# Optimization experiments

Measured on AMD Instinct MI355X. Metric: run time of the kernel, lower is better.

## Reference

```python
import jax, jax.numpy as jnp
import numpy as np

B, C, H, W = 2, 14, 128, 128
LOSS_WEIGHT = 0.5  # output = (1 - loss_weight) * sum of per-(bs,cls) log-Hausdorff losses
BIG = 1e6          # 'infinite' 1D distance for columns with no background pixel


def _edt_sq(is_zero):
    """Exact squared Euclidean distance transform of a [H,W] bool map.

    Returns, for every pixel, the squared distance to the nearest True pixel
    of `is_zero` (0 at True pixels). Matches scipy.ndimage.distance_transform_edt
    squared. Two-phase separable brute force (vectorized, no data loops).
    """
    h, w = is_zero.shape
    ii = jnp.arange(h, dtype=jnp.float32)
    absd = jnp.abs(ii[:, None] - ii[None, :])  # [H(i), H(p)] = |i - p|
    # d1[i, q] = min_{p : is_zero[p, q]} |i - p|   (per-column 1D distance)
    d1 = jnp.min(jnp.where(is_zero[None, :, :], absd[:, :, None], BIG), axis=1)  # [H, W]
    jj = jnp.arange(w, dtype=jnp.float32)
    off = (jj[:, None] - jj[None, :]) ** 2  # [W(q), W(j)] = (q - j)^2
    # sq[i, j] = min_q d1[i, q]^2 + (q - j)^2
    return jnp.min(d1[:, :, None] ** 2 + off[None, :, :], axis=1)  # [H, W]


def _distance_field_sq(img):
    """MONAI HausdorffDTLoss.distance_field squared: (edt(fg)+edt(bg))^2.

    fg_dist and bg_dist have disjoint supports, so (fg+bg)^2 = fg^2 + bg^2.
    Zero field if the image is all-foreground or all-background.
    """
    fg = img > 0.5
    field = _edt_sq(~fg) + _edt_sq(fg)
    valid = jnp.any(fg) & jnp.any(~fg)
    return jnp.where(valid, field, 0.0)


def _edge_mask(m):
    """mask XOR binary_erosion(mask): scipy default cross structuring element,
    border_value=0 (borders erode)."""
    p = jnp.pad(m, 1, constant_values=False)
    er = m & p[:-2, 1:-1] & p[2:, 1:-1] & p[1:-1, :-2] & p[1:-1, 2:]
    return m & ~er


def _pair_loss(stud_logit, seg_s, seg_t, teach_pred):
    # stud_logit: [H,W] float logits of this class; seg_s/seg_t: [H,W] bool
    # class masks; teach_pred: [H,W] teacher argmax labels (int)
    es = _edge_mask(seg_s).astype(stud_logit.dtype)
    et = _edge_mask(seg_t)
    pred = es * stud_logit                                      # edges * logits
    targ = jnp.where(et, teach_pred.astype(stud_logit.dtype), 0.0)  # edges * labels
    pred_dt2 = jax.lax.stop_gradient(_distance_field_sq(pred))  # MONAI detaches dt
    targ_dt2 = jax.lax.stop_gradient(_distance_field_sq(targ))
    hd = jnp.mean((pred - targ) ** 2 * (pred_dt2 + targ_dt2))   # alpha = 2
    return jnp.log(hd + 1.0)                                    # LogHausdorffDTLoss


def reference(logits_student, logits_teacher):
    ps = jnp.argmax(logits_student, axis=1)  # softmax is monotone -> argmax of logits
    pt = jnp.argmax(logits_teacher, axis=1)
    cls = jnp.arange(1, C)                   # classes 1..C-1 (background skipped)
    n = B * (C - 1)
    seg_s = (ps[:, None] == cls[None, :, None, None]).reshape(n, H, W)
    seg_t = (pt[:, None] == cls[None, :, None, None]).reshape(n, H, W)
    stud = logits_student[:, 1:].reshape(n, H, W)
    pt_rep = jnp.broadcast_to(pt[:, None], (B, C - 1, H, W)).reshape(n, H, W)
    losses = jax.vmap(_pair_loss)(stud, seg_s, seg_t, pt_rep)
    return (1.0 - LOSS_WEIGHT) * jnp.sum(losses)


def setup_inputs() -> dict:
    key = jax.random.key(0)
    k1, k2 = jax.random.split(key)
    return {
        "logits_student": jax.random.normal(k1, (B, C, H, W), dtype=jnp.float32),
        "logits_teacher": jax.random.normal(k2, (B, C, H, W), dtype=jnp.float32),
    }
```

## Files before the change

### kernel.cpp

```cpp
#include <hip/hip_runtime.h>
#include <math.h>
#include <limits.h>

#define HH 128
#define WW 128
#define HW (HH*WW)
#define BB 2
#define CC 14
#define NPAIR 26
#define RPB 8
#define NBLK (NPAIR * (HH / RPB))

typedef unsigned long long u64;


__device__ inline int nbd(u64 lo, u64 hi, int i) {
    int up = 255, down = 255;
    u64 slo, shi;
    if (i == 0)      { slo = lo; shi = hi; }
    else if (i < 64) { slo = (lo >> i) | (hi << (64 - i)); shi = hi >> i; }
    else             { slo = hi >> (i - 64); shi = 0ULL; }
    if (slo)      up = __builtin_ctzll(slo);
    else if (shi) up = 64 + __builtin_ctzll(shi);
    int s = 127 - i;
    u64 llo, lhi;
    if (s == 0)      { llo = lo; lhi = hi; }
    else if (s < 64) { lhi = (hi << s) | (lo >> (64 - s)); llo = lo << s; }
    else             { lhi = lo << (s - 64); llo = 0ULL; }
    if (lhi)      down = __builtin_clzll(lhi);
    else if (llo) down = 64 + __builtin_clzll(llo);
    return min(up, down);
}

__global__ void k_argmax(const float* __restrict__ Ls, const float* __restrict__ Lt,
                         unsigned char* __restrict__ ps, unsigned char* __restrict__ pt,
                         int* __restrict__ flags, float* __restrict__ sums,
                         int* __restrict__ done) {
    if (blockIdx.x == 0) {
        if (threadIdx.x < NPAIR) { flags[threadIdx.x] = 0; sums[threadIdx.x] = 0.0f; }
        if (threadIdx.x == 0) *done = 0;
    }
    int tid = blockIdx.x * blockDim.x + threadIdx.x;
    const int total4 = BB * HW / 4;
    if (tid >= 2 * total4) return;
    const float* L; unsigned char* dst; int p4;
    if (tid < total4) { L = Ls; dst = ps; p4 = tid; }
    else              { L = Lt; dst = pt; p4 = tid - total4; }
    int b = p4 / (HW / 4);
    int q4 = p4 - b * (HW / 4);
    const float4* base = (const float4*)(L + (size_t)b * CC * HW) + q4;
    float4 best = base[0];
    uchar4 bi = make_uchar4(0, 0, 0, 0);
#pragma unroll
    for (int c = 1; c < CC; ++c) {
        float4 v = base[(size_t)c * (HW / 4)];
        if (v.x > best.x) { best.x = v.x; bi.x = (unsigned char)c; }
        if (v.y > best.y) { best.y = v.y; bi.y = (unsigned char)c; }
        if (v.z > best.z) { best.z = v.z; bi.z = (unsigned char)c; }
        if (v.w > best.w) { best.w = v.w; bi.w = (unsigned char)c; }
    }
    ((uchar4*)dst)[b * (HW / 4) + q4] = bi;
}

__device__ inline u64 asm64(unsigned int (*p)[WW], int k0, int j) {
    return (u64)p[k0][j] | ((u64)p[k0 + 1][j] << 16)
         | ((u64)p[k0 + 2][j] << 32) | ((u64)p[k0 + 3][j] << 48);
}

__global__ __launch_bounds__(1024) void k_prep(
        const unsigned char* __restrict__ ps, const unsigned char* __restrict__ pt,
        const float* __restrict__ Ls,
        ulonglong2* __restrict__ cbP, ulonglong2* __restrict__ cbT,
        ulonglong2* __restrict__ esC, int* __restrict__ flags) {
    int n = blockIdx.x;
    int tid = threadIdx.x;
    int k = tid >> 7;
    int j = tid & (WW - 1);
    int b = n / (CC - 1), c = 1 + (n - b * (CC - 1));
    const unsigned char* P = ps + b * HW;
    const unsigned char* T = pt + b * HW;
    const float* Lp = Ls + (size_t)(b * CC + c) * HW;

    unsigned int s16 = 0, t16 = 0, h16 = 0;
    int i0 = k << 4;
#pragma unroll
    for (int r = 0; r < 16; ++r) {
        int off = (i0 + r) * WW + j;
        if (P[off] == c)      s16 |= 1u << r;
        if (T[off] == c)      t16 |= 1u << r;
        if (Lp[off] > 0.5f)   h16 |= 1u << r;
    }
    __shared__ unsigned int pS[8][WW], pT[8][WW], pH[8][WW];
    pS[k][j] = s16; pT[k][j] = t16; pH[k][j] = h16;
    __syncthreads();

    if (tid < WW) {
        u64 ms0 = asm64(pS, 0, j), ms1 = asm64(pS, 4, j);
        u64 mt0 = asm64(pT, 0, j), mt1 = asm64(pT, 4, j);
        u64 hi0 = asm64(pH, 0, j), hi1 = asm64(pH, 4, j);
        u64 Lsx = 0, Lsy = 0, Ltx = 0, Lty = 0, Rsx = 0, Rsy = 0, Rtx = 0, Rty = 0;
        if (j > 0)      { Lsx = asm64(pS, 0, j - 1); Lsy = asm64(pS, 4, j - 1);
                          Ltx = asm64(pT, 0, j - 1); Lty = asm64(pT, 4, j - 1); }
        if (j < WW - 1) { Rsx = asm64(pS, 0, j + 1); Rsy = asm64(pS, 4, j + 1);
                          Rtx = asm64(pT, 0, j + 1); Rty = asm64(pT, 4, j + 1); }

        u64 U0 = ms0 << 1, U1 = (ms1 << 1) | (ms0 >> 63);
        u64 D0 = (ms0 >> 1) | (ms1 << 63), D1 = ms1 >> 1;
        u64 er0 = ms0 & U0 & D0 & Lsx & Rsx;
        u64 er1 = ms1 & U1 & D1 & Lsy & Rsy;
        u64 es0 = ms0 & ~er0, es1 = ms1 & ~er1;

        u64 Ut0 = mt0 << 1, Ut1 = (mt1 << 1) | (mt0 >> 63);
        u64 Dt0 = (mt0 >> 1) | (mt1 << 63), Dt1 = mt1 >> 1;
        u64 ert0 = mt0 & Ut0 & Dt0 & Ltx & Rtx;
        u64 ert1 = mt1 & Ut1 & Dt1 & Lty & Rty;
        u64 et0 = mt0 & ~ert0, et1 = mt1 & ~ert1;

        u64 fp0 = es0 & hi0, fp1 = es1 & hi1;

        int idx = n * WW + j;
        cbP[idx] = make_ulonglong2(fp0, fp1);
        cbT[idx] = make_ulonglong2(et0, et1);
        esC[idx] = make_ulonglong2(es0, es1);

        u64 bFgP = __ballot((fp0 | fp1) != 0ull);
        u64 bBgP = __ballot((fp0 & fp1) != ~0ull);
        u64 bFgT = __ballot((et0 | et1) != 0ull);
        u64 bBgT = __ballot((et0 & et1) != ~0ull);
        if ((j & 63) == 0) {
            int fl = (bFgP ? 1 : 0) | (bBgP ? 2 : 0) | (bFgT ? 4 : 0) | (bBgT ? 8 : 0);
            atomicOr(&flags[n], fl);
        }
    }
}

__global__ __launch_bounds__(1024) void k_C(
        const float* __restrict__ Ls,
        const ulonglong2* __restrict__ cbP, const ulonglong2* __restrict__ cbT,
        const ulonglong2* __restrict__ esC,
        const int* __restrict__ flags, float* __restrict__ sums,
        int* __restrict__ done, float* __restrict__ out) {
    int n = blockIdx.x >> 4;
    int t = blockIdx.x & 15;
    int r = threadIdx.x >> 7;
    int j = threadIdx.x & (WW - 1);
    int i = t * RPB + r;
    int b = n / (CC - 1), c = 1 + (n - b * (CC - 1));

    int idx = n * WW + j;
    ulonglong2 mP = cbP[idx];
    ulonglong2 mT = cbT[idx];
    ulonglong2 eS = esC[idx];
    float lv = Ls[(size_t)(b * CC + c) * HW + i * WW + j];
    int f = flags[n];
    bool aP = (f & 3) == 3, aT = (f & 12) == 12;

    int dP  = nbd(mP.x, mP.y, i);
    int dPb = nbd(~mP.x, ~mP.y, i);
    int dT  = nbd(mT.x, mT.y, i);
    int dTb = nbd(~mT.x, ~mT.y, i);

    __shared__ uchar4 sq[RPB][WW];
    sq[r][j] = make_uchar4((unsigned char)dP, (unsigned char)dPb,
                           (unsigned char)dT, (unsigned char)dTb);
    __syncthreads();

    int bP = dP * dP, bPb = dPb * dPb, bT = dT * dT, bTb = dTb * dTb;
    int need = 0;
    if (aP) need = max(bP, bPb);
    if (aT) need = max(need, max(bT, bTb));
    for (int rad = 1; rad < WW; ++rad) {
        int rr = rad * rad;
        if (rr >= need) break;
        if (j >= rad) {
            uchar4 s = sq[r][j - rad];
            bP  = min(bP,  (int)s.x * s.x + rr); bPb = min(bPb, (int)s.y * s.y + rr);
            bT  = min(bT,  (int)s.z * s.z + rr); bTb = min(bTb, (int)s.w * s.w + rr);
        }
        if (j + rad < WW) {
            uchar4 s = sq[r][j + rad];
            bP  = min(bP,  (int)s.x * s.x + rr); bPb = min(bPb, (int)s.y * s.y + rr);
            bT  = min(bT,  (int)s.z * s.z + rr); bTb = min(bTb, (int)s.w * s.w + rr);
        }
        need = 0;
        if (aP) need = max(bP, bPb);
        if (aT) need = max(need, max(bT, bTb));
    }

    float fieldP = aP ? (float)(bP + bPb) : 0.0f;
    float fieldT = aT ? (float)(bT + bTb) : 0.0f;

    bool es = ((i < 64 ? (eS.x >> i) : (eS.y >> (i - 64))) & 1ull) != 0;
    bool et = ((i < 64 ? (mT.x >> i) : (mT.y >> (i - 64))) & 1ull) != 0;
    float predv = es ? lv : 0.0f;
    float targv = et ? (float)c : 0.0f;
    float diff = predv - targv;
    float v = diff * diff * (fieldP + fieldT);

    for (int o = 32; o > 0; o >>= 1) v += __shfl_down(v, o);
    __shared__ float wsum[16];
    __shared__ int won;
    int lane = threadIdx.x & 63, w = threadIdx.x >> 6;
    if (lane == 0) wsum[w] = v;
    if (threadIdx.x == 0) won = 0;
    __syncthreads();
    if (threadIdx.x == 0) {
        float tot = 0.0f;
#pragma unroll
        for (int q = 0; q < 16; ++q) tot += wsum[q];
        atomicAdd(&sums[n], tot);
        __threadfence();
        if (atomicAdd(done, 1) == NBLK - 1) won = 1;
    }
    __syncthreads();
    if (won && threadIdx.x < 64) {
        float vv = 0.0f;
        if (threadIdx.x < NPAIR) {
            float hd = atomicAdd(&sums[threadIdx.x], 0.0f) * (1.0f / (float)HW);
            vv = logf(hd + 1.0f);
        }
        for (int o = 32; o > 0; o >>= 1) vv += __shfl_down(vv, o);
        if (threadIdx.x == 0) out[0] = 0.5f * vv;
    }
}

extern "C" void kernel_launch(void* const* d_in, const int* in_sizes, int n_in,
                              void* d_out, int out_size, void* d_ws, size_t ws_size,
                              hipStream_t stream) {
    const float* Ls = (const float*)d_in[0];
    const float* Lt = (const float*)d_in[1];
    float* out = (float*)d_out;

    char* w = (char*)d_ws;
    unsigned char* ps    = (unsigned char*)(w);
    unsigned char* pt    = (unsigned char*)(w + 32768);
    ulonglong2*    cbP   = (ulonglong2*)   (w + 65536);
    ulonglong2*    cbT   = (ulonglong2*)   (w + 118784);
    ulonglong2*    esC   = (ulonglong2*)   (w + 172032);
    int*           flags = (int*)          (w + 225280);
    float*         sums  = (float*)        (w + 225408);
    int*           done  = (int*)          (w + 225536);

    k_argmax<<<(2 * BB * HW / 4 + 255) / 256, 256, 0, stream>>>(Ls, Lt, ps, pt, flags, sums, done);
    k_prep<<<NPAIR, 1024, 0, stream>>>(ps, pt, Ls, cbP, cbT, esC, flags);
    k_C<<<NBLK, 1024, 0, stream>>>(Ls, cbP, cbT, esC, flags, sums, done, out);
}
```

Baseline: 73.24 us.

## Fuse edge-mask prep into distance kernel, recomputing column bitmasks per block

Merges the per-pair prep kernel into the distance/loss kernel. Each of the 16 row-tile blocks per pair now rebuilds the column bitmasks (student/teacher edges, foreground) in shared memory and derives the validity flags locally instead of reading them from global memory. This removes one kernel launch, the global round trip for the masks and the flag atomics. In exchange, the mask-building work and its 128-row reads are repeated sixteen times per pair.

New measurement: 72.40 us. Within noise of the previous version (-1.1%).

```diff
diff --git a/kernel.cpp b/kernel.cpp
--- a/kernel.cpp
+++ b/kernel.cpp
@@ -34,10 +34,9 @@
 
 __global__ void k_argmax(const float* __restrict__ Ls, const float* __restrict__ Lt,
                          unsigned char* __restrict__ ps, unsigned char* __restrict__ pt,
-                         int* __restrict__ flags, float* __restrict__ sums,
-                         int* __restrict__ done) {
+                         float* __restrict__ sums, int* __restrict__ done) {
     if (blockIdx.x == 0) {
-        if (threadIdx.x < NPAIR) { flags[threadIdx.x] = 0; sums[threadIdx.x] = 0.0f; }
+        if (threadIdx.x < NPAIR) sums[threadIdx.x] = 0.0f;
         if (threadIdx.x == 0) *done = 0;
     }
     int tid = blockIdx.x * blockDim.x + threadIdx.x;
@@ -67,12 +66,12 @@
          | ((u64)p[k0 + 2][j] << 32) | ((u64)p[k0 + 3][j] << 48);
 }
 
-__global__ __launch_bounds__(1024) void k_prep(
+__global__ __launch_bounds__(1024) void k_C(
         const unsigned char* __restrict__ ps, const unsigned char* __restrict__ pt,
         const float* __restrict__ Ls,
-        ulonglong2* __restrict__ cbP, ulonglong2* __restrict__ cbT,
-        ulonglong2* __restrict__ esC, int* __restrict__ flags) {
-    int n = blockIdx.x;
+        float* __restrict__ sums, int* __restrict__ done, float* __restrict__ out) {
+    int n = blockIdx.x >> 4;
+    int t = blockIdx.x & 15;
     int tid = threadIdx.x;
     int k = tid >> 7;
     int j = tid & (WW - 1);
@@ -81,19 +80,24 @@
     const unsigned char* T = pt + b * HW;
     const float* Lp = Ls + (size_t)(b * CC + c) * HW;
 
+    int i = t * RPB + k;
+    float lv = Lp[i * WW + j];
+
     unsigned int s16 = 0, t16 = 0, h16 = 0;
     int i0 = k << 4;
 #pragma unroll
     for (int r = 0; r < 16; ++r) {
         int off = (i0 + r) * WW + j;
-        if (P[off] == c)      s16 |= 1u << r;
-        if (T[off] == c)      t16 |= 1u << r;
-        if (Lp[off] > 0.5f)   h16 |= 1u << r;
+        if (P[off] == c)              s16 |= 1u << r;
+        if (T[off] == c)              t16 |= 1u << r;
+        if (Lp[off] > 0.5f)           h16 |= 1u << r;
     }
     __shared__ unsigned int pS[8][WW], pT[8][WW], pH[8][WW];
     pS[k][j] = s16; pT[k][j] = t16; pH[k][j] = h16;
     __syncthreads();
 
+    __shared__ ulonglong2 colFP[WW], colET[WW], colES[WW];
+    __shared__ int sfl[2];
     if (tid < WW) {
         u64 ms0 = asm64(pS, 0, j), ms1 = asm64(pS, 4, j);
         u64 mt0 = asm64(pT, 0, j), mt1 = asm64(pT, 4, j);
@@ -118,41 +122,25 @@
 
         u64 fp0 = es0 & hi0, fp1 = es1 & hi1;
 
-        int idx = n * WW + j;
-        cbP[idx] = make_ulonglong2(fp0, fp1);
-        cbT[idx] = make_ulonglong2(et0, et1);
-        esC[idx] = make_ulonglong2(es0, es1);
+        colFP[j] = make_ulonglong2(fp0, fp1);
+        colET[j] = make_ulonglong2(et0, et1);
+        colES[j] = make_ulonglong2(es0, es1);
 
         u64 bFgP = __ballot((fp0 | fp1) != 0ull);
         u64 bBgP = __ballot((fp0 & fp1) != ~0ull);
         u64 bFgT = __ballot((et0 | et1) != 0ull);
         u64 bBgT = __ballot((et0 & et1) != ~0ull);
-        if ((j & 63) == 0) {
-            int fl = (bFgP ? 1 : 0) | (bBgP ? 2 : 0) | (bFgT ? 4 : 0) | (bBgT ? 8 : 0);
-            atomicOr(&flags[n], fl);
-        }
-    }
-}
-
-__global__ __launch_bounds__(1024) void k_C(
-        const float* __restrict__ Ls,
-        const ulonglong2* __restrict__ cbP, const ulonglong2* __restrict__ cbT,
-        const ulonglong2* __restrict__ esC,
-        const int* __restrict__ flags, float* __restrict__ sums,
-        int* __restrict__ done, float* __restrict__ out) {
-    int n = blockIdx.x >> 4;
-    int t = blockIdx.x & 15;
-    int r = threadIdx.x >> 7;
-    int j = threadIdx.x & (WW - 1);
-    int i = t * RPB + r;
-    int b = n / (CC - 1), c = 1 + (n - b * (CC - 1));
-
-    int idx = n * WW + j;
-    ulonglong2 mP = cbP[idx];
-    ulonglong2 mT = cbT[idx];
-    ulonglong2 eS = esC[idx];
-    float lv = Ls[(size_t)(b * CC + c) * HW + i * WW + j];
-    int f = flags[n];
+        if ((tid & 63) == 0) {
+            sfl[tid >> 6] = (bFgP ? 1 : 0) | (bBgP ? 2 : 0)
+                          | (bFgT ? 4 : 0) | (bBgT ? 8 : 0);
+        }
+    }
+    __syncthreads();
+
+    ulonglong2 mP = colFP[j];
+    ulonglong2 mT = colET[j];
+    ulonglong2 eS = colES[j];
+    int f = sfl[0] | sfl[1];
     bool aP = (f & 3) == 3, aT = (f & 12) == 12;
 
     int dP  = nbd(mP.x, mP.y, i);
@@ -161,7 +149,7 @@
     int dTb = nbd(~mT.x, ~mT.y, i);
 
     __shared__ uchar4 sq[RPB][WW];
-    sq[r][j] = make_uchar4((unsigned char)dP, (unsigned char)dPb,
+    sq[k][j] = make_uchar4((unsigned char)dP, (unsigned char)dPb,
                            (unsigned char)dT, (unsigned char)dTb);
     __syncthreads();
 
@@ -173,12 +161,12 @@
         int rr = rad * rad;
         if (rr >= need) break;
         if (j >= rad) {
-            uchar4 s = sq[r][j - rad];
+            uchar4 s = sq[k][j - rad];
             bP  = min(bP,  (int)s.x * s.x + rr); bPb = min(bPb, (int)s.y * s.y + rr);
             bT  = min(bT,  (int)s.z * s.z + rr); bTb = min(bTb, (int)s.w * s.w + rr);
         }
         if (j + rad < WW) {
-            uchar4 s = sq[r][j + rad];
+            uchar4 s = sq[k][j + rad];
             bP  = min(bP,  (int)s.x * s.x + rr); bPb = min(bPb, (int)s.y * s.y + rr);
             bT  = min(bT,  (int)s.z * s.z + rr); bTb = min(bTb, (int)s.w * s.w + rr);
         }
@@ -232,16 +220,11 @@
     float* out = (float*)d_out;
 
     char* w = (char*)d_ws;
-    unsigned char* ps    = (unsigned char*)(w);
-    unsigned char* pt    = (unsigned char*)(w + 32768);
-    ulonglong2*    cbP   = (ulonglong2*)   (w + 65536);
-    ulonglong2*    cbT   = (ulonglong2*)   (w + 118784);
-    ulonglong2*    esC   = (ulonglong2*)   (w + 172032);
-    int*           flags = (int*)          (w + 225280);
-    float*         sums  = (float*)        (w + 225408);
-    int*           done  = (int*)          (w + 225536);
-
-    k_argmax<<<(2 * BB * HW / 4 + 255) / 256, 256, 0, stream>>>(Ls, Lt, ps, pt, flags, sums, done);
-    k_prep<<<NPAIR, 1024, 0, stream>>>(ps, pt, Ls, cbP, cbT, esC, flags);
-    k_C<<<NBLK, 1024, 0, stream>>>(Ls, cbP, cbT, esC, flags, sums, done, out);
-}
+    unsigned char* ps   = (unsigned char*)(w);
+    unsigned char* pt   = (unsigned char*)(w + 32768);
+    float*         sums = (float*)        (w + 65536);
+    int*           done = (int*)          (w + 65664);
+
+    k_argmax<<<(2 * BB * HW / 4 + 255) / 256, 256, 0, stream>>>(Ls, Lt, ps, pt, sums, done);
+    k_C<<<NBLK, 1024, 0, stream>>>(ps, pt, Ls, sums, done, out);
+}
```
